# Performance work log

Measured on AMD Instinct MI355X. Metric: run time of the kernel, lower is better.

The kernel has to match this reference:

```python
import jax, jax.numpy as jnp
import numpy as np


def setup_inputs() -> dict:
    key = jax.random.key(0)
    k1, k2, k3 = jax.random.split(key, 3)
    B, N, M = 64, 1024, 1024
    src = jax.random.normal(k1, (B, 3, N), dtype=jnp.float32)
    tgt = jax.random.normal(k2, (B, 3, M), dtype=jnp.float32)
    scores = jax.random.normal(k3, (B, N, M), dtype=jnp.float32)
    return {"src": src, "tgt": tgt, "scores": scores}


def reference(src, tgt, scores):
    # softmax over the tgt-point axis (dim=2 in torch)
    p = jax.nn.softmax(scores, axis=2)                       # [B,N,M]
    # src_corr = tgt @ scores^T  -> soft correspondences in tgt for each src point
    src_corr = jnp.einsum('bdm,bnm->bdn', tgt, p)            # [B,3,N]
    src_mean = src.mean(axis=2, keepdims=True)               # [B,3,1]
    corr_mean = src_corr.mean(axis=2, keepdims=True)         # [B,3,1]
    src_c = src - src_mean
    corr_c = src_corr - corr_mean
    # cross-covariance H = src_centered @ src_corr_centered^T  -> [B,3,3]
    H = jnp.einsum('bdn,ben->bde', src_c, corr_c)
    U, S, Vh = jnp.linalg.svd(H)                             # batched 3x3 SVD
    V = jnp.swapaxes(Vh, -1, -2)
    Ut = jnp.swapaxes(U, -1, -2)
    R0 = V @ Ut                                              # candidate rotation
    det = jnp.linalg.det(R0)                                 # [B]
    # reflection fix: flip last column of V where det < 0 (reflect = diag(1,1,-1))
    flip = jnp.where(det < 0, -1.0, 1.0)                     # [B]
    ones = jnp.ones_like(flip)
    col_scale = jnp.stack([ones, ones, flip], axis=-1)[:, None, :]  # [B,1,3]
    R = (V * col_scale) @ Ut                                 # [B,3,3]
    t = (-R @ src_mean) + corr_mean                          # [B,3,1]
    return R, t.reshape(src.shape[0], 3)
```

## Files before the change

kernel.cpp:

```cpp
#include <hip/hip_runtime.h>
#include <math.h>

#define BATCH 64
#define NPTS  1024
#define MPTS  1024
#define WAVES_PER_BLOCK 8
#define ROWS_PER_BLOCK  WAVES_PER_BLOCK
#define BLOCKS_PER_BATCH (NPTS / ROWS_PER_BLOCK)
#define NBLOCKS (BATCH * BLOCKS_PER_BATCH)

typedef float f32x4 __attribute__((ext_vector_type(4)));

__global__ __launch_bounds__(512) void softmax_stats_kernel(
    const float* __restrict__ src,
    const float* __restrict__ tgt,
    const float* __restrict__ scores,
    float* __restrict__ partials)
{
    __shared__ float tgt_lds[3 * MPTS];
    __shared__ float part[WAVES_PER_BLOCK][16];

    const int tid  = threadIdx.x;
    const int lane = tid & 63;
    const int wave = tid >> 6;
    const int row0 = blockIdx.x * ROWS_PER_BLOCK;
    const int b    = row0 >> 10;
    const int r    = row0 + wave;
    const int n    = r & (NPTS - 1);

    const f32x4* srow = (const f32x4*)(scores + (size_t)r * MPTS);
    f32x4 v[4];
    #pragma unroll
    for (int k = 0; k < 4; ++k) v[k] = srow[k * 64 + lane];

    {
        const f32x4* tgt_g = (const f32x4*)(tgt + (size_t)b * 3 * MPTS);
        f32x4* tgt_l = (f32x4*)tgt_lds;
        int i1 = tid + 512;
        tgt_l[tid] = tgt_g[tid];
        if (i1 < 768) tgt_l[i1] = tgt_g[i1];
    }
    __syncthreads();

    float sum = 0.f, w0 = 0.f, w1 = 0.f, w2 = 0.f;
    #pragma unroll
    for (int k = 0; k < 4; ++k) {
        const int m4 = k * 64 + lane;
        float e0 = __expf(v[k].x);
        float e1 = __expf(v[k].y);
        float e2 = __expf(v[k].z);
        float e3 = __expf(v[k].w);
        sum += e0 + e1 + e2 + e3;
        f32x4 t0 = ((const f32x4*)(tgt_lds + 0 * MPTS))[m4];
        f32x4 t1 = ((const f32x4*)(tgt_lds + 1 * MPTS))[m4];
        f32x4 t2 = ((const f32x4*)(tgt_lds + 2 * MPTS))[m4];
        w0 += e0 * t0.x + e1 * t0.y + e2 * t0.z + e3 * t0.w;
        w1 += e0 * t1.x + e1 * t1.y + e2 * t1.z + e3 * t1.w;
        w2 += e0 * t2.x + e1 * t2.y + e2 * t2.z + e3 * t2.w;
    }
    #pragma unroll
    for (int off = 32; off >= 1; off >>= 1) {
        sum += __shfl_xor(sum, off);
        w0  += __shfl_xor(w0, off);
        w1  += __shfl_xor(w1, off);
        w2  += __shfl_xor(w2, off);
    }

    if (lane == 0) {
        const float inv = 1.0f / sum;
        const float c0 = w0 * inv, c1 = w1 * inv, c2 = w2 * inv;
        const float s0 = src[((size_t)b * 3 + 0) * NPTS + n];
        const float s1 = src[((size_t)b * 3 + 1) * NPTS + n];
        const float s2 = src[((size_t)b * 3 + 2) * NPTS + n];
        float* p = part[wave];
        p[0]  = s0; p[1]  = s1; p[2]  = s2;
        p[3]  = c0; p[4]  = c1; p[5]  = c2;
        p[6]  = s0 * c0; p[7]  = s0 * c1; p[8]  = s0 * c2;
        p[9]  = s1 * c0; p[10] = s1 * c1; p[11] = s1 * c2;
        p[12] = s2 * c0; p[13] = s2 * c1; p[14] = s2 * c2;
        p[15] = 0.f;
    }
    __syncthreads();

    if (tid < 16) {
        float a = 0.f;
        #pragma unroll
        for (int w = 0; w < WAVES_PER_BLOCK; ++w) a += part[w][tid];
        partials[(size_t)blockIdx.x * 16 + tid] = a;
    }
}

__global__ __launch_bounds__(64) void procrustes_kernel(
    const float* __restrict__ partials,
    float* __restrict__ out)
{
    const int b    = blockIdx.x;
    const int lane = threadIdx.x;

    float red = 0.f;
    #pragma unroll
    for (int j = 0; j < 32; ++j)
        red += partials[(size_t)b * 2048 + j * 64 + lane];
    red += __shfl_xor(red, 16);
    red += __shfl_xor(red, 32);
    float a[15];
    #pragma unroll
    for (int i = 0; i < 15; ++i) a[i] = __shfl(red, i);

    if (lane == 0) {
        const float invN = 1.0f / (float)NPTS;
        float mus[3], muc[3];
        #pragma unroll
        for (int d = 0; d < 3; ++d) { mus[d] = a[d] * invN; muc[d] = a[3 + d] * invN; }

        float Hm[3][3];
        #pragma unroll
        for (int d = 0; d < 3; ++d)
            #pragma unroll
            for (int e = 0; e < 3; ++e)
                Hm[d][e] = a[6 + d * 3 + e] - (float)NPTS * mus[d] * muc[e];

        float Bm[3][3], Vm[3][3];
        #pragma unroll
        for (int i = 0; i < 3; ++i)
            #pragma unroll
            for (int j = 0; j < 3; ++j) {
                Bm[i][j] = Hm[i][j];
                Vm[i][j] = (i == j) ? 1.f : 0.f;
            }

        const int PP[3] = {0, 0, 1};
        const int QQ[3] = {1, 2, 2};
        for (int sweep = 0; sweep < 8; ++sweep) {
            for (int rr = 0; rr < 3; ++rr) {
                const int p = PP[rr], q = QQ[rr];
                float aa = 0.f, bb = 0.f, c = 0.f;
                #pragma unroll
                for (int i = 0; i < 3; ++i) {
                    aa += Bm[i][p] * Bm[i][p];
                    bb += Bm[i][q] * Bm[i][q];
                    c  += Bm[i][p] * Bm[i][q];
                }
                if (fabsf(c) <= 1e-12f * sqrtf(aa * bb) || c == 0.f) continue;
                float tau = (bb - aa) / (2.f * c);
                float tt  = copysignf(1.f, tau) / (fabsf(tau) + sqrtf(1.f + tau * tau));
                float cs  = 1.f / sqrtf(1.f + tt * tt);
                float sn  = cs * tt;
                #pragma unroll
                for (int i = 0; i < 3; ++i) {
                    float bp = Bm[i][p], bq = Bm[i][q];
                    Bm[i][p] = cs * bp - sn * bq;
                    Bm[i][q] = sn * bp + cs * bq;
                    float vp = Vm[i][p], vq = Vm[i][q];
                    Vm[i][p] = cs * vp - sn * vq;
                    Vm[i][q] = sn * vp + cs * vq;
                }
            }
        }

        float sig[3];
        #pragma unroll
        for (int j = 0; j < 3; ++j)
            sig[j] = sqrtf(Bm[0][j] * Bm[0][j] + Bm[1][j] * Bm[1][j] + Bm[2][j] * Bm[2][j]);

        const int SP[3] = {0, 1, 0};
        const int SQ[3] = {1, 2, 1};
        for (int rr = 0; rr < 3; ++rr) {
            int p = SP[rr], q = SQ[rr];
            if (sig[p] < sig[q]) {
                float tsw = sig[p]; sig[p] = sig[q]; sig[q] = tsw;
                #pragma unroll
                for (int i = 0; i < 3; ++i) {
                    float t1 = Bm[i][p]; Bm[i][p] = Bm[i][q]; Bm[i][q] = t1;
                    float t2 = Vm[i][p]; Vm[i][p] = Vm[i][q]; Vm[i][q] = t2;
                }
            }
        }

        float Um[3][3];
        #pragma unroll
        for (int j = 0; j < 2; ++j) {
            float inv = 1.f / fmaxf(sig[j], 1e-30f);
            #pragma unroll
            for (int i = 0; i < 3; ++i) Um[i][j] = Bm[i][j] * inv;
        }
        if (sig[2] > 1e-6f * fmaxf(sig[0], 1e-30f)) {
            float inv = 1.f / sig[2];
            #pragma unroll
            for (int i = 0; i < 3; ++i) Um[i][2] = Bm[i][2] * inv;
        } else {
            float cx = Um[1][0] * Um[2][1] - Um[2][0] * Um[1][1];
            float cy = Um[2][0] * Um[0][1] - Um[0][0] * Um[2][1];
            float cz = Um[0][0] * Um[1][1] - Um[1][0] * Um[0][1];
            float inv = 1.f / fmaxf(sqrtf(cx * cx + cy * cy + cz * cz), 1e-30f);
            Um[0][2] = cx * inv; Um[1][2] = cy * inv; Um[2][2] = cz * inv;
        }

        float detU = Um[0][0] * (Um[1][1] * Um[2][2] - Um[1][2] * Um[2][1])
                   - Um[0][1] * (Um[1][0] * Um[2][2] - Um[1][2] * Um[2][0])
                   + Um[0][2] * (Um[1][0] * Um[2][1] - Um[1][1] * Um[2][0]);
        float detV = Vm[0][0] * (Vm[1][1] * Vm[2][2] - Vm[1][2] * Vm[2][1])
                   - Vm[0][1] * (Vm[1][0] * Vm[2][2] - Vm[1][2] * Vm[2][0])
                   + Vm[0][2] * (Vm[1][0] * Vm[2][1] - Vm[1][1] * Vm[2][0]);
        float flip = (detU * detV < 0.f) ? -1.f : 1.f;
        float fl[3] = {1.f, 1.f, flip};

        float R[3][3];
        #pragma unroll
        for (int i = 0; i < 3; ++i)
            #pragma unroll
            for (int j = 0; j < 3; ++j)
                R[i][j] = Vm[i][0] * fl[0] * Um[j][0]
                        + Vm[i][1] * fl[1] * Um[j][1]
                        + Vm[i][2] * fl[2] * Um[j][2];

        float* Rout = out + (size_t)b * 9;
        #pragma unroll
        for (int i = 0; i < 3; ++i)
            #pragma unroll
            for (int j = 0; j < 3; ++j)
                Rout[i * 3 + j] = R[i][j];

        float* tout = out + (size_t)BATCH * 9 + (size_t)b * 3;
        #pragma unroll
        for (int i = 0; i < 3; ++i)
            tout[i] = muc[i] - (R[i][0] * mus[0] + R[i][1] * mus[1] + R[i][2] * mus[2]);
    }
}

extern "C" void kernel_launch(void* const* d_in, const int* in_sizes, int n_in,
                              void* d_out, int out_size, void* d_ws, size_t ws_size,
                              hipStream_t stream) {
    const float* src    = (const float*)d_in[0];
    const float* tgt    = (const float*)d_in[1];
    const float* scores = (const float*)d_in[2];
    float* out      = (float*)d_out;
    float* partials = (float*)d_ws;

    softmax_stats_kernel<<<dim3(NBLOCKS), dim3(512), 0, stream>>>(
        src, tgt, scores, partials);

    procrustes_kernel<<<dim3(BATCH), dim3(64), 0, stream>>>(partials, out);
}
```

Baseline: 56.95 us.

## Drop LDS staging and block reduction; write per-row partials and reduce in second kernel

```diff
diff --git a/kernel.cpp b/kernel.cpp
--- a/kernel.cpp
+++ b/kernel.cpp
@@ -4,28 +4,23 @@
 #define BATCH 64
 #define NPTS  1024
 #define MPTS  1024
-#define WAVES_PER_BLOCK 8
-#define ROWS_PER_BLOCK  WAVES_PER_BLOCK
-#define BLOCKS_PER_BATCH (NPTS / ROWS_PER_BLOCK)
-#define NBLOCKS (BATCH * BLOCKS_PER_BATCH)
+#define WAVES_PER_BLOCK 4
+#define NROWS (BATCH * NPTS)
+#define NBLOCKS (NROWS / WAVES_PER_BLOCK)
 
 typedef float f32x4 __attribute__((ext_vector_type(4)));
 
-__global__ __launch_bounds__(512) void softmax_stats_kernel(
+__global__ __launch_bounds__(256) void softmax_stats_kernel(
     const float* __restrict__ src,
     const float* __restrict__ tgt,
     const float* __restrict__ scores,
     float* __restrict__ partials)
 {
-    __shared__ float tgt_lds[3 * MPTS];
-    __shared__ float part[WAVES_PER_BLOCK][16];
-
     const int tid  = threadIdx.x;
     const int lane = tid & 63;
     const int wave = tid >> 6;
-    const int row0 = blockIdx.x * ROWS_PER_BLOCK;
-    const int b    = row0 >> 10;
-    const int r    = row0 + wave;
+    const int r    = blockIdx.x * WAVES_PER_BLOCK + wave;
+    const int b    = r >> 10;
     const int n    = r & (NPTS - 1);
 
     const f32x4* srow = (const f32x4*)(scores + (size_t)r * MPTS);
@@ -33,30 +28,30 @@
     #pragma unroll
     for (int k = 0; k < 4; ++k) v[k] = srow[k * 64 + lane];
 
-    {
-        const f32x4* tgt_g = (const f32x4*)(tgt + (size_t)b * 3 * MPTS);
-        f32x4* tgt_l = (f32x4*)tgt_lds;
-        int i1 = tid + 512;
-        tgt_l[tid] = tgt_g[tid];
-        if (i1 < 768) tgt_l[i1] = tgt_g[i1];
-    }
-    __syncthreads();
+    const f32x4* tb = (const f32x4*)(tgt + (size_t)b * 3 * MPTS);
+    f32x4 tg0[4], tg1[4], tg2[4];
+    #pragma unroll
+    for (int k = 0; k < 4; ++k) tg0[k] = tb[0 * 256 + k * 64 + lane];
+    #pragma unroll
+    for (int k = 0; k < 4; ++k) tg1[k] = tb[1 * 256 + k * 64 + lane];
+    #pragma unroll
+    for (int k = 0; k < 4; ++k) tg2[k] = tb[2 * 256 + k * 64 + lane];
+
+    const float s0 = src[((size_t)b * 3 + 0) * NPTS + n];
+    const float s1 = src[((size_t)b * 3 + 1) * NPTS + n];
+    const float s2 = src[((size_t)b * 3 + 2) * NPTS + n];
 
     float sum = 0.f, w0 = 0.f, w1 = 0.f, w2 = 0.f;
     #pragma unroll
     for (int k = 0; k < 4; ++k) {
-        const int m4 = k * 64 + lane;
         float e0 = __expf(v[k].x);
         float e1 = __expf(v[k].y);
         float e2 = __expf(v[k].z);
         float e3 = __expf(v[k].w);
         sum += e0 + e1 + e2 + e3;
-        f32x4 t0 = ((const f32x4*)(tgt_lds + 0 * MPTS))[m4];
-        f32x4 t1 = ((const f32x4*)(tgt_lds + 1 * MPTS))[m4];
-        f32x4 t2 = ((const f32x4*)(tgt_lds + 2 * MPTS))[m4];
-        w0 += e0 * t0.x + e1 * t0.y + e2 * t0.z + e3 * t0.w;
-        w1 += e0 * t1.x + e1 * t1.y + e2 * t1.z + e3 * t1.w;
-        w2 += e0 * t2.x + e1 * t2.y + e2 * t2.z + e3 * t2.w;
+        w0 += e0 * tg0[k].x + e1 * tg0[k].y + e2 * tg0[k].z + e3 * tg0[k].w;
+        w1 += e0 * tg1[k].x + e1 * tg1[k].y + e2 * tg1[k].z + e3 * tg1[k].w;
+        w2 += e0 * tg2[k].x + e1 * tg2[k].y + e2 * tg2[k].z + e3 * tg2[k].w;
     }
     #pragma unroll
     for (int off = 32; off >= 1; off >>= 1) {
@@ -69,45 +64,42 @@
     if (lane == 0) {
         const float inv = 1.0f / sum;
         const float c0 = w0 * inv, c1 = w1 * inv, c2 = w2 * inv;
-        const float s0 = src[((size_t)b * 3 + 0) * NPTS + n];
-        const float s1 = src[((size_t)b * 3 + 1) * NPTS + n];
-        const float s2 = src[((size_t)b * 3 + 2) * NPTS + n];
-        float* p = part[wave];
-        p[0]  = s0; p[1]  = s1; p[2]  = s2;
-        p[3]  = c0; p[4]  = c1; p[5]  = c2;
-        p[6]  = s0 * c0; p[7]  = s0 * c1; p[8]  = s0 * c2;
-        p[9]  = s1 * c0; p[10] = s1 * c1; p[11] = s1 * c2;
-        p[12] = s2 * c0; p[13] = s2 * c1; p[14] = s2 * c2;
-        p[15] = 0.f;
-    }
-    __syncthreads();
-
-    if (tid < 16) {
-        float a = 0.f;
-        #pragma unroll
-        for (int w = 0; w < WAVES_PER_BLOCK; ++w) a += part[w][tid];
-        partials[(size_t)blockIdx.x * 16 + tid] = a;
+        f32x4* p = (f32x4*)(partials + (size_t)r * 16);
+        f32x4 q0 = {s0, s1, s2, c0};
+        f32x4 q1 = {c1, c2, s0 * c0, s0 * c1};
+        f32x4 q2 = {s0 * c2, s1 * c0, s1 * c1, s1 * c2};
+        f32x4 q3 = {s2 * c0, s2 * c1, s2 * c2, 0.f};
+        p[0] = q0; p[1] = q1; p[2] = q2; p[3] = q3;
     }
 }
 
-__global__ __launch_bounds__(64) void procrustes_kernel(
+__global__ __launch_bounds__(256) void procrustes_kernel(
     const float* __restrict__ partials,
     float* __restrict__ out)
 {
+    __shared__ float wlds[4][16];
+
     const int b    = blockIdx.x;
-    const int lane = threadIdx.x;
-
-    float red = 0.f;
-    #pragma unroll
-    for (int j = 0; j < 32; ++j)
-        red += partials[(size_t)b * 2048 + j * 64 + lane];
-    red += __shfl_xor(red, 16);
-    red += __shfl_xor(red, 32);
-    float a[15];
-    #pragma unroll
-    for (int i = 0; i < 15; ++i) a[i] = __shfl(red, i);
-
-    if (lane == 0) {
+    const int tid  = threadIdx.x;
+    const int lane = tid & 63;
+    const int wave = tid >> 6;
+
+    float acc = 0.f;
+    const float* pb = partials + (size_t)b * 16384;
+    #pragma unroll 8
+    for (int j = 0; j < 64; ++j)
+        acc += pb[j * 256 + tid];
+    acc += __shfl_xor(acc, 16);
+    acc += __shfl_xor(acc, 32);
+    if (lane < 16) wlds[wave][lane] = acc;
+    __syncthreads();
+
+    if (tid == 0) {
+        float a[15];
+        #pragma unroll
+        for (int i = 0; i < 15; ++i)
+            a[i] = wlds[0][i] + wlds[1][i] + wlds[2][i] + wlds[3][i];
+
         const float invN = 1.0f / (float)NPTS;
         float mus[3], muc[3];
         #pragma unroll
@@ -237,8 +229,8 @@
     float* out      = (float*)d_out;
     float* partials = (float*)d_ws;
 
-    softmax_stats_kernel<<<dim3(NBLOCKS), dim3(512), 0, stream>>>(
+    softmax_stats_kernel<<<dim3(NBLOCKS), dim3(256), 0, stream>>>(
         src, tgt, scores, partials);
 
-    procrustes_kernel<<<dim3(BATCH), dim3(64), 0, stream>>>(partials, out);
+    procrustes_kernel<<<dim3(BATCH), dim3(256), 0, stream>>>(partials, out);
 }
```

Result: slower. 65.44 us (+14.9%).
